# Kernel tuning notes

Hardware: AMD Instinct MI355X
Metric: run time of the kernel (lower is better)

Reference implementation:

```python
import jax, jax.numpy as jnp
import numpy as np

HID, NH, L, BS, WLEN = 768, 12, 512, 16, 2048
AD = HID // NH
EPS = 1e-5


def _counts_front(wn, L):
    # torch: _, count = wn.unique(return_counts=True); counts[:len(count)] += count
    # i.e. bincount compacted: counts of sorted unique values placed at the FRONT.
    c = jnp.zeros((L,), jnp.float32).at[wn].add(1.0)          # bincount over node ids
    nz = c > 0
    pos = jnp.cumsum(nz.astype(jnp.int32)) - 1                # destination slot per nonzero
    idx = jnp.where(nz, pos, L)                               # out-of-range -> dropped
    return jnp.zeros((L,), jnp.float32).at[idx].add(c, mode='drop')


def setup_inputs() -> dict:
    key = jax.random.key(0)
    ks = jax.random.split(key, 16)
    s = 1.0 / np.sqrt(HID)
    return {
        'x': jax.random.normal(ks[0], (BS, L, HID), jnp.float32),
        'attn_bias': jax.random.normal(ks[1], (BS, NH, L, L), jnp.float32),
        'walk_nodes': jax.random.randint(ks[2], (BS, WLEN), 0, L),
        'n_nodes': jax.random.randint(ks[3], (BS,), 0, L),
        'ln_g': jnp.ones((HID,), jnp.float32),
        'ln_b': jnp.zeros((HID,), jnp.float32),
        'Wq': jax.random.normal(ks[4], (HID, HID), jnp.float32) * s,
        'bq': jnp.zeros((HID,), jnp.float32),
        'Wk': jax.random.normal(ks[5], (HID, HID), jnp.float32) * s,
        'bk': jnp.zeros((HID,), jnp.float32),
        'Wv': jax.random.normal(ks[6], (HID, HID), jnp.float32) * s,
        'bv': jnp.zeros((HID,), jnp.float32),
        'Wo': jax.random.normal(ks[7], (HID, HID), jnp.float32) * s,
        'bo': jnp.zeros((HID,), jnp.float32),
    }


def reference(x, attn_bias, walk_nodes, n_nodes, ln_g, ln_b, Wq, bq, Wk, bk, Wv, bv, Wo, bo):
    bs, Lx, _ = x.shape
    # LayerNorm
    mu = jnp.mean(x, -1, keepdims=True)
    var = jnp.mean((x - mu) ** 2, -1, keepdims=True)
    xn = (x - mu) * jax.lax.rsqrt(var + EPS) * ln_g + ln_b
    q = (xn @ Wq + bq).reshape(bs, Lx, NH, AD)
    k = (xn @ Wk + bk).reshape(bs, Lx, NH, AD)
    v = (xn @ Wv + bv).reshape(bs, Lx, NH, AD)
    # per-token V reweighting from walk-node counts
    counts = jax.vmap(lambda wn: _counts_front(wn, Lx))(walk_nodes)  # [bs, L]
    weight = counts / walk_nodes.shape[1] * n_nodes.astype(jnp.float32)[:, None]
    v = v * weight[:, :, None, None]
    scale = AD ** (-0.5)
    attn = jnp.einsum('bqhd,bkhd->bhqk', q, k) * scale + attn_bias
    attn = jax.nn.softmax(attn, axis=-1)
    out = jnp.einsum('bhqk,bkhd->bqhd', attn, v).reshape(bs, Lx, NH * AD)
    return out @ Wo + bo
```

## Files before the change

kernel.cpp:

```cpp
#include <hip/hip_runtime.h>

#define HID 768
#define NH 12
#define LSEQ 512
#define BS 16
#define WLEN 2048
#define AD 64

typedef unsigned short u16;
typedef short short8 __attribute__((ext_vector_type(8)));
typedef float f32x4 __attribute__((ext_vector_type(4)));

#define MFMA16(a, b, c) __builtin_amdgcn_mfma_f32_16x16x32_bf16((a), (b), (c), 0, 0, 0)

__device__ __forceinline__ u16 f2bf(float f) {
  union { float f; unsigned u; } v; v.f = f;
  unsigned u = v.u;
  return (u16)((u + 0x7fffu + ((u >> 16) & 1u)) >> 16);
}

__global__ __launch_bounds__(256) void transpose_kernel(const float* __restrict__ W,
                                                        u16* __restrict__ dst) {
  __shared__ float tile[64][65];
  const int k0 = blockIdx.x * 64, n0 = blockIdx.y * 64;
  for (int i = threadIdx.x; i < 64 * 64; i += 256) {
    const int r = i >> 6, c = i & 63;
    tile[r][c] = W[(size_t)(k0 + r) * HID + n0 + c];
  }
  __syncthreads();
  for (int i = threadIdx.x; i < 64 * 64; i += 256) {
    const int r = i >> 6, c = i & 63;
    dst[(size_t)(n0 + r) * HID + k0 + c] = f2bf(tile[c][r]);
  }
}

__global__ __launch_bounds__(512) void counts_kernel(const int* __restrict__ wn,
                                                     const int* __restrict__ nn,
                                                     float* __restrict__ wgt) {
  __shared__ int cnt[LSEQ];
  __shared__ int sc[2][LSEQ];
  const int b = blockIdx.x, t = threadIdx.x;
  cnt[t] = 0;
  __syncthreads();
  for (int i = t; i < WLEN; i += 512) atomicAdd(&cnt[wn[b * WLEN + i]], 1);
  __syncthreads();
  const int c = cnt[t];
  const int nz = c > 0 ? 1 : 0;
  sc[0][t] = nz;
  __syncthreads();
  int src = 0;
  for (int step = 1; step < LSEQ; step <<= 1) {
    int v = sc[src][t];
    if (t >= step) v += sc[src][t - step];
    sc[src ^ 1][t] = v;
    __syncthreads();
    src ^= 1;
  }
  wgt[b * LSEQ + t] = 0.0f;
  __syncthreads();
  if (nz) {
    const int slot = sc[src][t] - 1;
    wgt[b * LSEQ + slot] = (float)c * (float)nn[b] * (1.0f / WLEN);
  }
}

__global__ __launch_bounds__(256) void ln_kernel(const float* __restrict__ x,
                                                 const float* __restrict__ g,
                                                 const float* __restrict__ bb,
                                                 u16* __restrict__ xn) {
  const int w = threadIdx.x >> 6, lane = threadIdx.x & 63;
  const int row = blockIdx.x * 4 + w;
  const float* xr = x + (size_t)row * HID + lane * 12;
  float4 v0 = *(const float4*)(xr);
  float4 v1 = *(const float4*)(xr + 4);
  float4 v2 = *(const float4*)(xr + 8);
  float vv[12] = {v0.x, v0.y, v0.z, v0.w, v1.x, v1.y, v1.z, v1.w, v2.x, v2.y, v2.z, v2.w};
  float s = 0.f, q = 0.f;
#pragma unroll
  for (int j = 0; j < 12; ++j) { s += vv[j]; q += vv[j] * vv[j]; }
#pragma unroll
  for (int d = 1; d < 64; d <<= 1) { s += __shfl_xor(s, d); q += __shfl_xor(q, d); }
  const float mean = s * (1.0f / HID);
  const float var = q * (1.0f / HID) - mean * mean;
  const float rs = rsqrtf(var + 1e-5f);
  const float* gp = g + lane * 12;
  const float* bp = bb + lane * 12;
  unsigned pk[6];
#pragma unroll
  for (int j = 0; j < 6; ++j) {
    const u16 lo = f2bf((vv[2 * j] - mean) * rs * gp[2 * j] + bp[2 * j]);
    const u16 hi = f2bf((vv[2 * j + 1] - mean) * rs * gp[2 * j + 1] + bp[2 * j + 1]);
    pk[j] = (unsigned)lo | ((unsigned)hi << 16);
  }
  unsigned* dst = (unsigned*)(xn + (size_t)row * HID + lane * 12);
#pragma unroll
  for (int j = 0; j < 6; ++j) dst[j] = pk[j];
}

template <int MODE>
__global__ __launch_bounds__(256) void gemm_kernel(
    const u16* __restrict__ A, const u16* __restrict__ Bt,
    const float* __restrict__ bias0, const float* __restrict__ bias1,
    const float* __restrict__ bias2, const float* __restrict__ wgt,
    u16* __restrict__ qb, u16* __restrict__ kb, u16* __restrict__ vt,
    float* __restrict__ outf) {
  __shared__ u16 at[128][40];
  __shared__ u16 bt[128][40];
  const int tid = threadIdx.x;
  const int lane = tid & 63, w = tid >> 6;
  const int wr = w >> 1, wc = w & 1;
  const int fr = lane & 15, fc = lane >> 4;
  const int row0 = blockIdx.x * 128, col0 = blockIdx.y * 128;

  const f32x4 zero4 = {0.f, 0.f, 0.f, 0.f};
  f32x4 acc[4][4];
#pragma unroll
  for (int m = 0; m < 4; ++m)
#pragma unroll
    for (int n = 0; n < 4; ++n) acc[m][n] = zero4;

  const int srow = tid >> 1, soff = (tid & 1) * 16;
  const u16* aptr = A + (size_t)(row0 + srow) * HID + soff;
  const u16* bptr = Bt + (size_t)(col0 + srow) * HID + soff;

  for (int kt = 0; kt < HID / 32; ++kt) {
    const short8 a0 = *(const short8*)(aptr);
    const short8 a1 = *(const short8*)(aptr + 8);
    const short8 b0 = *(const short8*)(bptr);
    const short8 b1 = *(const short8*)(bptr + 8);
    aptr += 32; bptr += 32;
    __syncthreads();
    *(short8*)&at[srow][soff] = a0;
    *(short8*)&at[srow][soff + 8] = a1;
    *(short8*)&bt[srow][soff] = b0;
    *(short8*)&bt[srow][soff + 8] = b1;
    __syncthreads();
    short8 af[4], bfr[4];
#pragma unroll
    for (int m = 0; m < 4; ++m) af[m] = *(const short8*)&at[wr * 64 + m * 16 + fr][fc * 8];
#pragma unroll
    for (int n = 0; n < 4; ++n) bfr[n] = *(const short8*)&bt[wc * 64 + n * 16 + fr][fc * 8];
#pragma unroll
    for (int m = 0; m < 4; ++m)
#pragma unroll
      for (int n = 0; n < 4; ++n)
        acc[m][n] = MFMA16(af[m], bfr[n], acc[m][n]);
  }

  if (MODE == 0) {
    const int reg = col0 / HID;
    const float* bias = (reg == 0) ? bias0 : (reg == 1) ? bias1 : bias2;
#pragma unroll
    for (int m = 0; m < 4; ++m) {
      const int row = row0 + wr * 64 + m * 16 + fc * 4;
      const int b = row >> 9;
      const int tok0 = row & 511;
#pragma unroll
      for (int n = 0; n < 4; ++n) {
        const int cc = (col0 - reg * HID) + wc * 64 + n * 16 + fr;
        const int h = cc >> 6, d = cc & 63;
        const float bval = bias[cc];
#pragma unroll
        for (int r = 0; r < 4; ++r) {
          const float v = acc[m][n][r] + bval;
          const int tok = tok0 + r;
          if (reg == 0)
            qb[(((size_t)b * NH + h) * LSEQ + tok) * AD + d] = f2bf(v * 0.125f);
          else if (reg == 1)
            kb[(((size_t)b * NH + h) * LSEQ + tok) * AD + d] = f2bf(v);
          else
            vt[(((size_t)b * NH + h) * AD + d) * LSEQ + tok] = f2bf(v * wgt[b * LSEQ + tok]);
        }
      }
    }
  } else {
#pragma unroll
    for (int m = 0; m < 4; ++m) {
      const int row = row0 + wr * 64 + m * 16 + fc * 4;
#pragma unroll
      for (int n = 0; n < 4; ++n) {
        const int col = col0 + wc * 64 + n * 16 + fr;
        const float bval = bias0[col];
#pragma unroll
        for (int r = 0; r < 4; ++r)
          outf[(size_t)(row + r) * HID + col] = acc[m][n][r] + bval;
      }
    }
  }
}

__global__ __launch_bounds__(256) void attn_kernel(const u16* __restrict__ qb,
                                                   const u16* __restrict__ kb,
                                                   const u16* __restrict__ vt,
                                                   const float* __restrict__ bias,
                                                   u16* __restrict__ aout) {
  __shared__ u16 p_lds[4][16][72];
  const int tid = threadIdx.x;
  const int w = tid >> 6, lane = tid & 63;
  const int fr = lane & 15, fc = lane >> 4;
  const int blk = blockIdx.x;
  const int qt = blk & 7, bh = blk >> 3;
  const int h = bh % NH, b = bh / NH;
  const int q0 = qt * 64 + w * 16;

  const u16* qbase = qb + (size_t)bh * LSEQ * AD;
  const u16* kbase = kb + (size_t)bh * LSEQ * AD;
  const u16* vbase = vt + (size_t)bh * AD * LSEQ;
  const float* bbase = bias + (size_t)bh * LSEQ * LSEQ;

  const short8 aq0 = *(const short8*)(qbase + (size_t)(q0 + fr) * AD + fc * 8);
  const short8 aq1 = *(const short8*)(qbase + (size_t)(q0 + fr) * AD + 32 + fc * 8);

  const f32x4 zero4 = {0.f, 0.f, 0.f, 0.f};
  f32x4 o[4];
  float m_r[4], l_r[4];
#pragma unroll
  for (int f = 0; f < 4; ++f) o[f] = zero4;
#pragma unroll
  for (int r = 0; r < 4; ++r) { m_r[r] = -3.0e38f; l_r[r] = 0.f; }

  for (int kt = 0; kt < 8; ++kt) {
    const int kv0 = kt * 64;
    f32x4 s[4];
#pragma unroll
    for (int f = 0; f < 4; ++f) {
      const float* bp = bbase + (size_t)(q0 + fc * 4) * LSEQ + kv0 + f * 16 + fr;
#pragma unroll
      for (int r = 0; r < 4; ++r) s[f][r] = bp[(size_t)r * LSEQ];
    }
#pragma unroll
    for (int f = 0; f < 4; ++f) {
      const u16* kp = kbase + (size_t)(kv0 + f * 16 + fr) * AD + fc * 8;
      const short8 k0v = *(const short8*)kp;
      const short8 k1v = *(const short8*)(kp + 32);
      s[f] = MFMA16(aq0, k0v, s[f]);
      s[f] = MFMA16(aq1, k1v, s[f]);
    }
    float alpha[4];
#pragma unroll
    for (int r = 0; r < 4; ++r) {
      float mx = fmaxf(fmaxf(s[0][r], s[1][r]), fmaxf(s[2][r], s[3][r]));
#pragma unroll
      for (int d = 1; d < 16; d <<= 1) mx = fmaxf(mx, __shfl_xor(mx, d));
      const float mn = fmaxf(m_r[r], mx);
      alpha[r] = __expf(m_r[r] - mn);
      m_r[r] = mn;
      float ps = 0.f;
#pragma unroll
      for (int f = 0; f < 4; ++f) {
        const float p = __expf(s[f][r] - mn);
        s[f][r] = p;
        ps += p;
      }
#pragma unroll
      for (int d = 1; d < 16; d <<= 1) ps += __shfl_xor(ps, d);
      l_r[r] = l_r[r] * alpha[r] + ps;
    }
#pragma unroll
    for (int f = 0; f < 4; ++f)
#pragma unroll
      for (int r = 0; r < 4; ++r) o[f][r] *= alpha[r];
#pragma unroll
    for (int f = 0; f < 4; ++f)
#pragma unroll
      for (int r = 0; r < 4; ++r) p_lds[w][fc * 4 + r][f * 16 + fr] = f2bf(s[f][r]);
    const short8 pa0 = *(const short8*)&p_lds[w][fr][fc * 8];
    const short8 pa1 = *(const short8*)&p_lds[w][fr][32 + fc * 8];
#pragma unroll
    for (int f = 0; f < 4; ++f) {
      const u16* vp = vbase + (size_t)(f * 16 + fr) * LSEQ + kv0 + fc * 8;
      const short8 v0 = *(const short8*)vp;
      const short8 v1 = *(const short8*)(vp + 32);
      o[f] = MFMA16(pa0, v0, o[f]);
      o[f] = MFMA16(pa1, v1, o[f]);
    }
  }
#pragma unroll
  for (int f = 0; f < 4; ++f)
#pragma unroll
    for (int r = 0; r < 4; ++r) {
      const float val = o[f][r] / l_r[r];
      const int row = b * LSEQ + q0 + fc * 4 + r;
      const int col = h * AD + f * 16 + fr;
      aout[(size_t)row * HID + col] = f2bf(val);
    }
}

extern "C" void kernel_launch(void* const* d_in, const int* in_sizes, int n_in,
                              void* d_out, int out_size, void* d_ws, size_t ws_size,
                              hipStream_t stream) {
  const float* x = (const float*)d_in[0];
  const float* bias = (const float*)d_in[1];
  const int* wn = (const int*)d_in[2];
  const int* nn = (const int*)d_in[3];
  const float* lng = (const float*)d_in[4];
  const float* lnb = (const float*)d_in[5];
  const float* Wq = (const float*)d_in[6];
  const float* bq = (const float*)d_in[7];
  const float* Wk = (const float*)d_in[8];
  const float* bk = (const float*)d_in[9];
  const float* Wv = (const float*)d_in[10];
  const float* bv = (const float*)d_in[11];
  const float* Wo = (const float*)d_in[12];
  const float* bo = (const float*)d_in[13];
  float* out = (float*)d_out;

  char* ws = (char*)d_ws;
  float* wgt = (float*)ws;
  u16* xn = (u16*)(ws + 32768);
  u16* wt = xn + (size_t)8192 * 768;
  u16* wot = wt + (size_t)2304 * 768;
  u16* qb = wot + (size_t)768 * 768;
  u16* kb = qb + (size_t)BS * NH * LSEQ * AD;
  u16* vt = kb + (size_t)BS * NH * LSEQ * AD;
  u16* aout = xn;

  hipLaunchKernelGGL(transpose_kernel, dim3(12, 12), dim3(256), 0, stream, Wq, wt);
  hipLaunchKernelGGL(transpose_kernel, dim3(12, 12), dim3(256), 0, stream, Wk,
                     wt + (size_t)768 * 768);
  hipLaunchKernelGGL(transpose_kernel, dim3(12, 12), dim3(256), 0, stream, Wv,
                     wt + (size_t)2 * 768 * 768);
  hipLaunchKernelGGL(transpose_kernel, dim3(12, 12), dim3(256), 0, stream, Wo, wot);
  hipLaunchKernelGGL(counts_kernel, dim3(BS), dim3(512), 0, stream, wn, nn, wgt);
  hipLaunchKernelGGL(ln_kernel, dim3(2048), dim3(256), 0, stream, x, lng, lnb, xn);
  hipLaunchKernelGGL((gemm_kernel<0>), dim3(64, 18), dim3(256), 0, stream, xn, wt, bq, bk,
                     bv, wgt, qb, kb, vt, (float*)nullptr);
  hipLaunchKernelGGL(attn_kernel, dim3(1536), dim3(256), 0, stream, qb, kb, vt, bias, aout);
  hipLaunchKernelGGL((gemm_kernel<1>), dim3(64, 6), dim3(256), 0, stream, aout, wot, bo,
                     (const float*)nullptr, (const float*)nullptr, (const float*)nullptr,
                     (u16*)nullptr, (u16*)nullptr, (u16*)nullptr, out);
}
```

Measured before the change: 506.2 us.

## Use direct global-to-LDS loads, LDS-staged epilogues, transposed QK MFMA and prefetched bias

The GEMM now stages its A and B tiles with global_load_lds into an XOR-swizzled LDS layout. Its epilogues go through LDS so Q, K and output writes are vectorised and coalesced, and V^T writes are packed. The attention kernel computes K·Q^T so each lane holds contiguous bias columns, which are loaded as float4 and prefetched one tile ahead. Softmax row statistics now need only two shuffles, and the block order is remapped to group heads. The four weight transposes are merged into one launch. Together these target uncoalesced bias and epilogue traffic and launch overhead, at the cost of extra LDS use and added register pressure.

```diff
diff --git a/kernel.cpp b/kernel.cpp
--- a/kernel.cpp
+++ b/kernel.cpp
@@ -8,20 +8,32 @@
 #define AD 64
 
 typedef unsigned short u16;
+typedef unsigned int u32;
 typedef short short8 __attribute__((ext_vector_type(8)));
 typedef float f32x4 __attribute__((ext_vector_type(4)));
 
 #define MFMA16(a, b, c) __builtin_amdgcn_mfma_f32_16x16x32_bf16((a), (b), (c), 0, 0, 0)
 
 __device__ __forceinline__ u16 f2bf(float f) {
-  union { float f; unsigned u; } v; v.f = f;
-  unsigned u = v.u;
+  union { float f; u32 u; } v; v.f = f;
+  u32 u = v.u;
   return (u16)((u + 0x7fffu + ((u >> 16) & 1u)) >> 16);
 }
 
-__global__ __launch_bounds__(256) void transpose_kernel(const float* __restrict__ W,
-                                                        u16* __restrict__ dst) {
+__device__ __forceinline__ void gload16(const u16* g, u16* l) {
+  __builtin_amdgcn_global_load_lds(
+      (const __attribute__((address_space(1))) u32*)g,
+      (__attribute__((address_space(3))) u32*)l, 16, 0, 0);
+}
+
+__global__ __launch_bounds__(256) void transpose4_kernel(
+    const float* __restrict__ Wq, const float* __restrict__ Wk,
+    const float* __restrict__ Wv, const float* __restrict__ Wo,
+    u16* __restrict__ wt, u16* __restrict__ wot) {
   __shared__ float tile[64][65];
+  const int z = blockIdx.z;
+  const float* W = (z == 0) ? Wq : (z == 1) ? Wk : (z == 2) ? Wv : Wo;
+  u16* dst = (z < 3) ? (wt + (size_t)z * HID * HID) : wot;
   const int k0 = blockIdx.x * 64, n0 = blockIdx.y * 64;
   for (int i = threadIdx.x; i < 64 * 64; i += 256) {
     const int r = i >> 6, c = i & 63;
@@ -85,14 +97,14 @@
   const float rs = rsqrtf(var + 1e-5f);
   const float* gp = g + lane * 12;
   const float* bp = bb + lane * 12;
-  unsigned pk[6];
+  u32 pk[6];
 #pragma unroll
   for (int j = 0; j < 6; ++j) {
     const u16 lo = f2bf((vv[2 * j] - mean) * rs * gp[2 * j] + bp[2 * j]);
     const u16 hi = f2bf((vv[2 * j + 1] - mean) * rs * gp[2 * j + 1] + bp[2 * j + 1]);
-    pk[j] = (unsigned)lo | ((unsigned)hi << 16);
-  }
-  unsigned* dst = (unsigned*)(xn + (size_t)row * HID + lane * 12);
+    pk[j] = (u32)lo | ((u32)hi << 16);
+  }
+  u32* dst = (u32*)(xn + (size_t)row * HID + lane * 12);
 #pragma unroll
   for (int j = 0; j < 6; ++j) dst[j] = pk[j];
 }
@@ -104,86 +116,119 @@
     const float* __restrict__ bias2, const float* __restrict__ wgt,
     u16* __restrict__ qb, u16* __restrict__ kb, u16* __restrict__ vt,
     float* __restrict__ outf) {
-  __shared__ u16 at[128][40];
-  __shared__ u16 bt[128][40];
+  __shared__ __align__(16) char smem[17408];
+  u16* at = (u16*)smem;
+  u16* bt = at + 128 * 32;
   const int tid = threadIdx.x;
   const int lane = tid & 63, w = tid >> 6;
   const int wr = w >> 1, wc = w & 1;
   const int fr = lane & 15, fc = lane >> 4;
   const int row0 = blockIdx.x * 128, col0 = blockIdx.y * 128;
 
-  const f32x4 zero4 = {0.f, 0.f, 0.f, 0.f};
   f32x4 acc[4][4];
 #pragma unroll
   for (int m = 0; m < 4; ++m)
 #pragma unroll
-    for (int n = 0; n < 4; ++n) acc[m][n] = zero4;
-
-  const int srow = tid >> 1, soff = (tid & 1) * 16;
-  const u16* aptr = A + (size_t)(row0 + srow) * HID + soff;
-  const u16* bptr = Bt + (size_t)(col0 + srow) * HID + soff;
+    for (int n = 0; n < 4; ++n) acc[m][n] = (f32x4){0.f, 0.f, 0.f, 0.f};
+
+  const int csrc = (((lane & 3) ^ ((lane >> 3) & 3))) * 8;
+  const int lrow = lane >> 2;
+  const u16* aS0 = A + (size_t)(row0 + w * 16 + lrow) * HID + csrc;
+  const u16* aS1 = A + (size_t)(row0 + 64 + w * 16 + lrow) * HID + csrc;
+  const u16* bS0 = Bt + (size_t)(col0 + w * 16 + lrow) * HID + csrc;
+  const u16* bS1 = Bt + (size_t)(col0 + 64 + w * 16 + lrow) * HID + csrc;
+  u16* atd0 = at + (w * 16) * 32;
+  u16* atd1 = at + (64 + w * 16) * 32;
+  u16* btd0 = bt + (w * 16) * 32;
+  u16* btd1 = bt + (64 + w * 16) * 32;
+  const int axor = (fc ^ ((fr >> 1) & 3)) * 8;
 
   for (int kt = 0; kt < HID / 32; ++kt) {
-    const short8 a0 = *(const short8*)(aptr);
-    const short8 a1 = *(const short8*)(aptr + 8);
-    const short8 b0 = *(const short8*)(bptr);
-    const short8 b1 = *(const short8*)(bptr + 8);
-    aptr += 32; bptr += 32;
     __syncthreads();
-    *(short8*)&at[srow][soff] = a0;
-    *(short8*)&at[srow][soff + 8] = a1;
-    *(short8*)&bt[srow][soff] = b0;
-    *(short8*)&bt[srow][soff + 8] = b1;
+    gload16(aS0, atd0); gload16(aS1, atd1);
+    gload16(bS0, btd0); gload16(bS1, btd1);
+    aS0 += 32; aS1 += 32; bS0 += 32; bS1 += 32;
     __syncthreads();
     short8 af[4], bfr[4];
 #pragma unroll
-    for (int m = 0; m < 4; ++m) af[m] = *(const short8*)&at[wr * 64 + m * 16 + fr][fc * 8];
-#pragma unroll
-    for (int n = 0; n < 4; ++n) bfr[n] = *(const short8*)&bt[wc * 64 + n * 16 + fr][fc * 8];
-#pragma unroll
     for (int m = 0; m < 4; ++m)
-#pragma unroll
-      for (int n = 0; n < 4; ++n)
-        acc[m][n] = MFMA16(af[m], bfr[n], acc[m][n]);
-  }
+      af[m] = *(const short8*)(at + (wr * 64 + m * 16 + fr) * 32 + axor);
+#pragma unroll
+    for (int n = 0; n < 4; ++n)
+      bfr[n] = *(const short8*)(bt + (wc * 64 + n * 16 + fr) * 32 + axor);
+#pragma unroll
+    for (int m = 0; m < 4; ++m)
+#pragma unroll
+      for (int n = 0; n < 4; ++n) acc[m][n] = MFMA16(af[m], bfr[n], acc[m][n]);
+  }
+
+  __syncthreads();
 
   if (MODE == 0) {
-    const int reg = col0 / HID;
+    const int reg = blockIdx.y / 6;
+    const int cloc = (blockIdx.y % 6) * 128;
+    const int b = row0 >> 9;
+    const int tok_base = (row0 & 511) + wr * 64;
+    const int hh = ((cloc + wc * 64) >> 6);
     const float* bias = (reg == 0) ? bias0 : (reg == 1) ? bias1 : bias2;
+    if (reg == 2) {
+#pragma unroll
+      for (int m = 0; m < 4; ++m) {
+        const int tok0 = tok_base + m * 16 + fc * 4;
+        const f32x4 wv = *(const f32x4*)&wgt[b * LSEQ + tok0];
+#pragma unroll
+        for (int n = 0; n < 4; ++n) {
+          const int d = n * 16 + fr;
+          const float bval = bias[cloc + wc * 64 + d];
+          const u32 p0 = (u32)f2bf((acc[m][n][0] + bval) * wv[0]) |
+                         ((u32)f2bf((acc[m][n][1] + bval) * wv[1]) << 16);
+          const u32 p1 = (u32)f2bf((acc[m][n][2] + bval) * wv[2]) |
+                         ((u32)f2bf((acc[m][n][3] + bval) * wv[3]) << 16);
+          u16* dp = vt + (((size_t)(b * NH + hh) * AD + d) * LSEQ + tok0);
+          *(uint2*)dp = make_uint2(p0, p1);
+        }
+      }
+    } else {
+      u16* dst = (reg == 0) ? qb : kb;
+      const float scl = (reg == 0) ? 0.125f : 1.0f;
+      u16* rw = (u16*)smem + w * (16 * 72);
+#pragma unroll
+      for (int m = 0; m < 4; ++m) {
+#pragma unroll
+        for (int n = 0; n < 4; ++n) {
+          const float bval = bias[cloc + wc * 64 + n * 16 + fr];
+#pragma unroll
+          for (int r = 0; r < 4; ++r)
+            rw[(fc * 4 + r) * 72 + n * 16 + fr] = f2bf((acc[m][n][r] + bval) * scl);
+        }
+#pragma unroll
+        for (int p = 0; p < 2; ++p) {
+          const int rr = p * 8 + (lane >> 3);
+          const int doff = (lane & 7) * 8;
+          const short8 vv = *(const short8*)&rw[rr * 72 + doff];
+          const int tok = tok_base + m * 16 + rr;
+          *(short8*)(dst + ((size_t)(b * NH + hh) * LSEQ + tok) * AD + doff) = vv;
+        }
+      }
+    }
+  } else {
+    float* rwf = (float*)smem + w * (16 * 68);
 #pragma unroll
     for (int m = 0; m < 4; ++m) {
-      const int row = row0 + wr * 64 + m * 16 + fc * 4;
-      const int b = row >> 9;
-      const int tok0 = row & 511;
 #pragma unroll
       for (int n = 0; n < 4; ++n) {
-        const int cc = (col0 - reg * HID) + wc * 64 + n * 16 + fr;
-        const int h = cc >> 6, d = cc & 63;
-        const float bval = bias[cc];
-#pragma unroll
-        for (int r = 0; r < 4; ++r) {
-          const float v = acc[m][n][r] + bval;
-          const int tok = tok0 + r;
-          if (reg == 0)
-            qb[(((size_t)b * NH + h) * LSEQ + tok) * AD + d] = f2bf(v * 0.125f);
-          else if (reg == 1)
-            kb[(((size_t)b * NH + h) * LSEQ + tok) * AD + d] = f2bf(v);
-          else
-            vt[(((size_t)b * NH + h) * AD + d) * LSEQ + tok] = f2bf(v * wgt[b * LSEQ + tok]);
-        }
-      }
-    }
-  } else {
-#pragma unroll
-    for (int m = 0; m < 4; ++m) {
-      const int row = row0 + wr * 64 + m * 16 + fc * 4;
-#pragma unroll
-      for (int n = 0; n < 4; ++n) {
-        const int col = col0 + wc * 64 + n * 16 + fr;
-        const float bval = bias0[col];
+        const float bval = bias0[col0 + wc * 64 + n * 16 + fr];
 #pragma unroll
         for (int r = 0; r < 4; ++r)
-          outf[(size_t)(row + r) * HID + col] = acc[m][n][r] + bval;
+          rwf[(fc * 4 + r) * 68 + n * 16 + fr] = acc[m][n][r] + bval;
+      }
+#pragma unroll
+      for (int p = 0; p < 4; ++p) {
+        const int rr = p * 4 + (lane >> 4);
+        const int c4 = (lane & 15) * 4;
+        const float4 v = *(const float4*)&rwf[rr * 68 + c4];
+        const int row = row0 + wr * 64 + m * 16 + rr;
+        *(float4*)&outf[(size_t)row * HID + col0 + wc * 64 + c4] = v;
       }
     }
   }
@@ -194,76 +239,83 @@
                                                    const u16* __restrict__ vt,
                                                    const float* __restrict__ bias,
                                                    u16* __restrict__ aout) {
-  __shared__ u16 p_lds[4][16][72];
+  __shared__ __align__(16) u16 p_lds[4][16][72];
   const int tid = threadIdx.x;
   const int w = tid >> 6, lane = tid & 63;
   const int fr = lane & 15, fc = lane >> 4;
-  const int blk = blockIdx.x;
-  const int qt = blk & 7, bh = blk >> 3;
+  const int x = blockIdx.x;
+  const int bh = (x & 7) | ((x >> 6) << 3);
+  const int qt = (x >> 3) & 7;
   const int h = bh % NH, b = bh / NH;
   const int q0 = qt * 64 + w * 16;
 
   const u16* qbase = qb + (size_t)bh * LSEQ * AD;
   const u16* kbase = kb + (size_t)bh * LSEQ * AD;
   const u16* vbase = vt + (size_t)bh * AD * LSEQ;
-  const float* bbase = bias + (size_t)bh * LSEQ * LSEQ;
+  const float* brow = bias + (size_t)bh * LSEQ * LSEQ + (size_t)(q0 + fr) * LSEQ + fc * 4;
 
   const short8 aq0 = *(const short8*)(qbase + (size_t)(q0 + fr) * AD + fc * 8);
   const short8 aq1 = *(const short8*)(qbase + (size_t)(q0 + fr) * AD + 32 + fc * 8);
 
-  const f32x4 zero4 = {0.f, 0.f, 0.f, 0.f};
   f32x4 o[4];
-  float m_r[4], l_r[4];
-#pragma unroll
-  for (int f = 0; f < 4; ++f) o[f] = zero4;
-#pragma unroll
-  for (int r = 0; r < 4; ++r) { m_r[r] = -3.0e38f; l_r[r] = 0.f; }
+#pragma unroll
+  for (int f = 0; f < 4; ++f) o[f] = (f32x4){0.f, 0.f, 0.f, 0.f};
+  float m_r = -3.0e38f, l_r = 0.f;
+
+  f32x4 bc[4];
+#pragma unroll
+  for (int f = 0; f < 4; ++f) bc[f] = *(const f32x4*)(brow + f * 16);
 
   for (int kt = 0; kt < 8; ++kt) {
     const int kv0 = kt * 64;
     f32x4 s[4];
 #pragma unroll
-    for (int f = 0; f < 4; ++f) {
-      const float* bp = bbase + (size_t)(q0 + fc * 4) * LSEQ + kv0 + f * 16 + fr;
-#pragma unroll
-      for (int r = 0; r < 4; ++r) s[f][r] = bp[(size_t)r * LSEQ];
+    for (int f = 0; f < 4; ++f) s[f] = bc[f];
+    if (kt < 7) {
+#pragma unroll
+      for (int f = 0; f < 4; ++f) bc[f] = *(const f32x4*)(brow + (kt + 1) * 64 + f * 16);
     }
 #pragma unroll
     for (int f = 0; f < 4; ++f) {
       const u16* kp = kbase + (size_t)(kv0 + f * 16 + fr) * AD + fc * 8;
-      const short8 k0v = *(const short8*)kp;
-      const short8 k1v = *(const short8*)(kp + 32);
-      s[f] = MFMA16(aq0, k0v, s[f]);
-      s[f] = MFMA16(aq1, k1v, s[f]);
-    }
-    float alpha[4];
-#pragma unroll
-    for (int r = 0; r < 4; ++r) {
-      float mx = fmaxf(fmaxf(s[0][r], s[1][r]), fmaxf(s[2][r], s[3][r]));
-#pragma unroll
-      for (int d = 1; d < 16; d <<= 1) mx = fmaxf(mx, __shfl_xor(mx, d));
-      const float mn = fmaxf(m_r[r], mx);
-      alpha[r] = __expf(m_r[r] - mn);
-      m_r[r] = mn;
-      float ps = 0.f;
-#pragma unroll
-      for (int f = 0; f < 4; ++f) {
+      const short8 k0 = *(const short8*)kp;
+      const short8 k1 = *(const short8*)(kp + 32);
+      s[f] = MFMA16(k0, aq0, s[f]);
+      s[f] = MFMA16(k1, aq1, s[f]);
+    }
+    float mx = s[0][0];
+#pragma unroll
+    for (int f = 0; f < 4; ++f)
+#pragma unroll
+      for (int r = 0; r < 4; ++r) mx = fmaxf(mx, s[f][r]);
+    mx = fmaxf(mx, __shfl_xor(mx, 16));
+    mx = fmaxf(mx, __shfl_xor(mx, 32));
+    const float mn = fmaxf(m_r, mx);
+    const float alpha = __expf(m_r - mn);
+    m_r = mn;
+    float ps = 0.f;
+#pragma unroll
+    for (int f = 0; f < 4; ++f)
+#pragma unroll
+      for (int r = 0; r < 4; ++r) {
         const float p = __expf(s[f][r] - mn);
         s[f][r] = p;
         ps += p;
       }
-#pragma unroll
-      for (int d = 1; d < 16; d <<= 1) ps += __shfl_xor(ps, d);
-      l_r[r] = l_r[r] * alpha[r] + ps;
-    }
+    l_r = l_r * alpha + ps;
+    float arow[4];
+#pragma unroll
+    for (int r = 0; r < 4; ++r) arow[r] = __shfl(alpha, fc * 4 + r);
 #pragma unroll
     for (int f = 0; f < 4; ++f)
 #pragma unroll
-      for (int r = 0; r < 4; ++r) o[f][r] *= alpha[r];
-#pragma unroll
-    for (int f = 0; f < 4; ++f)
-#pragma unroll
-      for (int r = 0; r < 4; ++r) p_lds[w][fc * 4 + r][f * 16 + fr] = f2bf(s[f][r]);
+      for (int r = 0; r < 4; ++r) o[f][r] *= arow[r];
+#pragma unroll
+    for (int f = 0; f < 4; ++f) {
+      const u32 p0 = (u32)f2bf(s[f][0]) | ((u32)f2bf(s[f][1]) << 16);
+      const u32 p1 = (u32)f2bf(s[f][2]) | ((u32)f2bf(s[f][3]) << 16);
+      *(uint2*)&p_lds[w][fr][f * 16 + fc * 4] = make_uint2(p0, p1);
+    }
     const short8 pa0 = *(const short8*)&p_lds[w][fr][fc * 8];
     const short8 pa1 = *(const short8*)&p_lds[w][fr][32 + fc * 8];
 #pragma unroll
@@ -275,14 +327,19 @@
       o[f] = MFMA16(pa1, v1, o[f]);
     }
   }
+  float l_tot = l_r;
+  l_tot += __shfl_xor(l_tot, 16);
+  l_tot += __shfl_xor(l_tot, 32);
+  float rinv[4];
+#pragma unroll
+  for (int r = 0; r < 4; ++r) rinv[r] = 1.0f / __shfl(l_tot, fc * 4 + r);
 #pragma unroll
   for (int f = 0; f < 4; ++f)
 #pragma unroll
     for (int r = 0; r < 4; ++r) {
-      const float val = o[f][r] / l_r[r];
       const int row = b * LSEQ + q0 + fc * 4 + r;
       const int col = h * AD + f * 16 + fr;
-      aout[(size_t)row * HID + col] = f2bf(val);
+      aout[(size_t)row * HID + col] = f2bf(o[f][r] * rinv[r]);
     }
 }
 
@@ -315,18 +372,15 @@
   u16* vt = kb + (size_t)BS * NH * LSEQ * AD;
   u16* aout = xn;
 
-  hipLaunchKernelGGL(transpose_kernel, dim3(12, 12), dim3(256), 0, stream, Wq, wt);
-  hipLaunchKernelGGL(transpose_kernel, dim3(12, 12), dim3(256), 0, stream, Wk,
-                     wt + (size_t)768 * 768);
-  hipLaunchKernelGGL(transpose_kernel, dim3(12, 12), dim3(256), 0, stream, Wv,
-                     wt + (size_t)2 * 768 * 768);
-  hipLaunchKernelGGL(transpose_kernel, dim3(12, 12), dim3(256), 0, stream, Wo, wot);
+  hipLaunchKernelGGL(transpose4_kernel, dim3(12, 12, 4), dim3(256), 0, stream,
+                     Wq, Wk, Wv, Wo, wt, wot);
   hipLaunchKernelGGL(counts_kernel, dim3(BS), dim3(512), 0, stream, wn, nn, wgt);
   hipLaunchKernelGGL(ln_kernel, dim3(2048), dim3(256), 0, stream, x, lng, lnb, xn);
-  hipLaunchKernelGGL((gemm_kernel<0>), dim3(64, 18), dim3(256), 0, stream, xn, wt, bq, bk,
-                     bv, wgt, qb, kb, vt, (float*)nullptr);
+  hipLaunchKernelGGL((gemm_kernel<0>), dim3(64, 18), dim3(256), 0, stream, xn, wt,
+                     bq, bk, bv, wgt, qb, kb, vt, (float*)nullptr);
   hipLaunchKernelGGL(attn_kernel, dim3(1536), dim3(256), 0, stream, qb, kb, vt, bias, aout);
-  hipLaunchKernelGGL((gemm_kernel<1>), dim3(64, 6), dim3(256), 0, stream, aout, wot, bo,
-                     (const float*)nullptr, (const float*)nullptr, (const float*)nullptr,
-                     (u16*)nullptr, (u16*)nullptr, (u16*)nullptr, out);
-}
+  hipLaunchKernelGGL((gemm_kernel<1>), dim3(64, 6), dim3(256), 0, stream, aout, wot,
+                     bo, (const float*)nullptr, (const float*)nullptr,
+                     (const float*)nullptr, (u16*)nullptr, (u16*)nullptr,
+                     (u16*)nullptr, out);
+}
```

Result: faster. 473.1 us (-6.5%).
